# Kernel optimization log

Hardware: AMD Instinct MI355X
Metric: run time of the kernel (lower is better)

Reference implementation:

```python
import jax, jax.numpy as jnp
import numpy as np

B, SEQ, S, DIM_IN, DIM_K, DIM_V = 4, 2048, 128, 512, 64, 64
L = SEQ + 2 * S
NEG = -1e30  # stand-in for log(0) in the tril mask (finite for stable vjp)


def _layernorm(x, g, b, eps=1e-5):
    m = jnp.mean(x, axis=-1, keepdims=True)
    v = jnp.var(x, axis=-1, keepdims=True)
    return (x - m) / jnp.sqrt(v + eps) * g + b


def setup_inputs() -> dict:
    key = jax.random.key(0)
    ks = jax.random.split(key, 18)
    w = lambda k, shape, s=0.02: (jax.random.normal(k, shape, jnp.float32) * s)
    inp = {
        "x": jax.random.normal(ks[0], (B, L, DIM_IN), jnp.float32),
        "Wq": w(ks[1], (DIM_IN, DIM_K)),
        "Wk": w(ks[2], (DIM_IN, DIM_K)),
        "Wv": w(ks[3], (DIM_IN, DIM_V)),
        "Wq_s": w(ks[4], (DIM_IN, DIM_K)),
        "Wk_s": w(ks[5], (DIM_IN, DIM_K)),
        "Wv_s": w(ks[6], (DIM_IN, DIM_V)),
        "Wq_e": w(ks[7], (DIM_IN, DIM_K)),
        "Wk_e": w(ks[8], (DIM_IN, DIM_K)),
        "Wv_e": w(ks[9], (DIM_IN, DIM_V)),
        "ln_g": jnp.ones((DIM_IN,), jnp.float32),
        "ln_b": jnp.zeros((DIM_IN,), jnp.float32),
        "ln_s_g": jnp.ones((DIM_IN,), jnp.float32),
        "ln_s_b": jnp.zeros((DIM_IN,), jnp.float32),
        "ln_e_g": jnp.ones((DIM_IN,), jnp.float32),
        "ln_e_b": jnp.zeros((DIM_IN,), jnp.float32),
        "cope_emb": jax.random.normal(ks[10], (DIM_K, S), jnp.float32),
        "offset": 0,
    }
    return inp


def reference(x, Wq, Wk, Wv, Wq_s, Wk_s, Wv_s, Wq_e, Wk_e, Wv_e,
              ln_g, ln_b, ln_s_g, ln_s_b, ln_e_g, ln_e_b, cope_emb, offset):
    # extract_state: first/last state_len tokens
    xs, xm, xe = x[:, :S], x[:, S:L - S], x[:, -S:]
    xm = _layernorm(xm, ln_g, ln_b)
    xs = _layernorm(xs, ln_s_g, ln_s_b)
    xe = _layernorm(xe, ln_e_g, ln_e_b)

    q, k, v = xm @ Wq, xm @ Wk, xm @ Wv          # (B, SEQ, dk/dv)
    q_s, k_s, v_s = xs @ Wq_s, xs @ Wk_s, xs @ Wv_s
    q_e, k_e, v_e = xe @ Wq_e, xe @ Wk_e, xe @ Wv_e

    # CoPE bias over the non-state block
    logits = jnp.einsum('bqd,bkd->bqk', q, k)    # (B, SEQ, SEQ)
    gates = jax.nn.sigmoid(logits)
    pos = jnp.flip(jnp.cumsum(jnp.flip(gates, -1), axis=-1), -1)
    pos = jnp.minimum(pos, jnp.float32(S - 1))
    pos_ceil = jnp.ceil(pos).astype(jnp.int32)
    pos_floor = jnp.floor(pos).astype(jnp.int32)
    logits_int = jnp.einsum('bqd,dk->bqk', q, cope_emb)  # (B, SEQ, S)
    logits_c = jnp.take_along_axis(logits_int, pos_ceil, axis=-1)
    logits_f = jnp.take_along_axis(logits_int, pos_floor, axis=-1)
    wfrac = pos - pos_floor.astype(pos.dtype)
    bias = logits_c * wfrac + logits_f * (1.0 - wfrac)   # (B, SEQ, SEQ)

    q_full = jnp.concatenate([q_s, q, q_e], axis=1)      # (B, L, dk)
    k_full = jnp.concatenate([k_s, k, k_e], axis=1)
    v_full = jnp.concatenate([v_s, v, v_e], axis=1)

    # explicit tril log-mask bias with CoPE injected in the middle block
    tri = jnp.tril(jnp.ones((L, L), dtype=bool))
    attn_bias = jnp.where(tri, 0.0, NEG).astype(jnp.float32)
    attn_bias = jnp.broadcast_to(attn_bias, (B, L, L))
    attn_bias = attn_bias.at[:, S:L - S, S:L - S].add(bias)

    scale = 1.0 / jnp.sqrt(jnp.float32(DIM_K))
    scores = jnp.einsum('bqd,bkd->bqk', q_full, k_full) * scale + attn_bias
    att = jax.nn.softmax(scores, axis=-1)
    return jnp.einsum('bqk,bkd->bqd', att, v_full)       # (B, L, dv)
```

## Files before the change

kernel.cpp:

```cpp
#include <hip/hip_runtime.h>
#include <math.h>

#define B_    4
#define SEQ_  2048
#define S_    128
#define L_    2304
#define DIN   512
#define DK    64
#define NEGINF (-1e30f)
#define SCALE 0.125f
#define NCOLS 2176
#define NMID  8192
#define NEDGE 1024
#define LE    2304

typedef _Float16 f16;
typedef __attribute__((ext_vector_type(8))) _Float16 half8;
typedef __attribute__((ext_vector_type(4))) float f32x4;

union U4 { uint4 u; f16 h[8]; half8 v; };

__global__ __launch_bounds__(256) void k_wsplit(
    const float* __restrict__ Wq,  const float* __restrict__ Wk,  const float* __restrict__ Wv,
    const float* __restrict__ Wqs, const float* __restrict__ Wks, const float* __restrict__ Wvs,
    const float* __restrict__ Wqe, const float* __restrict__ Wke, const float* __restrict__ Wve,
    f16* __restrict__ Wsp)
{
    __shared__ float xs[64 * 68];
    const int kt  = blockIdx.x;
    const int mat = blockIdx.y;
    const float* W;
    switch (mat) {
        case 0: W = Wq;  break; case 1: W = Wk;  break; case 2: W = Wv;  break;
        case 3: W = Wqs; break; case 4: W = Wks; break; case 5: W = Wvs; break;
        case 6: W = Wqe; break; case 7: W = Wke; break; default: W = Wve; break;
    }
    const int tid = threadIdx.x;
    const int k0  = kt * 64;
    #pragma unroll
    for (int i = 0; i < 4; ++i) {
        int g = tid + 256 * i;
        int k = g >> 4, c4 = g & 15;
        *(float4*)(xs + k * 68 + c4 * 4) = ((const float4*)W)[(size_t)(k0 + k) * 16 + c4];
    }
    __syncthreads();
    const int col = tid & 63, hf = tid >> 6;
    const int kk0 = hf * 16;
    U4 hi0, hi1, lo0, lo1;
    #pragma unroll
    for (int j = 0; j < 8; ++j) {
        float v0 = xs[(kk0 + j) * 68 + col];
        float v1 = xs[(kk0 + 8 + j) * 68 + col];
        hi0.h[j] = (f16)v0; lo0.h[j] = (f16)(v0 - (float)hi0.h[j]);
        hi1.h[j] = (f16)v1; lo1.h[j] = (f16)(v1 - (float)hi1.h[j]);
    }
    f16* dst = Wsp + (size_t)mat * 65536 + (size_t)col * 1024 + k0 + kk0;
    *(uint4*)(dst)       = hi0.u;
    *(uint4*)(dst + 8)   = hi1.u;
    *(uint4*)(dst + 512) = lo0.u;
    *(uint4*)(dst + 520) = lo1.u;
}

__global__ __launch_bounds__(256) void k_proj(
    const float* __restrict__ x, const f16* __restrict__ Wsp,
    const float* __restrict__ g0, const float* __restrict__ b0,
    const float* __restrict__ gs, const float* __restrict__ bs,
    const float* __restrict__ ge, const float* __restrict__ be,
    f16* __restrict__ qsp, f16* __restrict__ ksp, f16* __restrict__ vhT)
{
    __shared__ f16 Bs[3 * 64 * 136];
    __shared__ float mean_s[32], rstd_s[32];
    const int tid  = threadIdx.x;
    const int row0 = blockIdx.x * 32;
    const int rseq = row0 % L_;
    const int seg  = (rseq < S_) ? 0 : (rseq >= L_ - S_) ? 2 : 1;
    const int mat0 = (seg == 0) ? 3 : (seg == 2) ? 6 : 0;
    const float* gg = (seg == 0) ? gs : (seg == 2) ? ge : g0;
    const float* bb = (seg == 0) ? bs : (seg == 2) ? be : b0;

    {
        const int rr = tid >> 3, qq = tid & 7;
        const float4* xr = (const float4*)(x + (size_t)(row0 + rr) * DIN) + qq * 16;
        float s = 0.f, s2 = 0.f;
        #pragma unroll
        for (int i = 0; i < 16; ++i) {
            float4 v = xr[i];
            s  += v.x + v.y + v.z + v.w;
            s2 += v.x * v.x + v.y * v.y + v.z * v.z + v.w * v.w;
        }
        s  += __shfl_xor(s, 1);  s  += __shfl_xor(s, 2);  s  += __shfl_xor(s, 4);
        s2 += __shfl_xor(s2, 1); s2 += __shfl_xor(s2, 2); s2 += __shfl_xor(s2, 4);
        if (qq == 0) {
            float mean = s * (1.f / DIN);
            mean_s[rr] = mean;
            rstd_s[rr] = rsqrtf(s2 * (1.f / DIN) - mean * mean + 1e-5f);
        }
    }

    const int w = tid >> 6, lane = tid & 63;
    const int cl = lane & 15, quad = lane >> 4;
    const int r0 = 16 * (w >> 1), c0 = 32 * (w & 1);

    f32x4 acc[3][2];
    #pragma unroll
    for (int m = 0; m < 3; ++m)
        #pragma unroll
        for (int j = 0; j < 2; ++j) acc[m][j] = 0.f;

    const int arow = row0 + r0 + cl;

    for (int kc = 0; kc < DIN; kc += 64) {
        __syncthreads();
        #pragma unroll
        for (int i = 0; i < 6; ++i) {
            int g = tid + 256 * i;
            int mm = g >> 9, rem = g & 511;
            int col = rem >> 3, c8 = rem & 7;
            const f16* src = Wsp + (size_t)(mat0 + mm) * 65536 + (size_t)col * 1024 + kc + c8 * 8;
            f16* dst = Bs + mm * 8704 + col * 136 + c8 * 8;
            *(uint4*)(dst)      = *(const uint4*)(src);
            *(uint4*)(dst + 64) = *(const uint4*)(src + 512);
        }
        __syncthreads();
        const float mean = mean_s[r0 + cl], rstd = rstd_s[r0 + cl];
        #pragma unroll
        for (int h = 0; h < 2; ++h) {
            const float* xp = x + (size_t)arow * DIN + kc + h * 32 + quad * 8;
            float4 a0 = *(const float4*)xp;
            float4 a1 = *(const float4*)(xp + 4);
            const float* gp = gg + kc + h * 32 + quad * 8;
            const float* bp = bb + kc + h * 32 + quad * 8;
            float4 gA = *(const float4*)gp, gB = *(const float4*)(gp + 4);
            float4 bA = *(const float4*)bp, bB = *(const float4*)(bp + 4);
            float n[8];
            n[0] = (a0.x - mean) * rstd * gA.x + bA.x;
            n[1] = (a0.y - mean) * rstd * gA.y + bA.y;
            n[2] = (a0.z - mean) * rstd * gA.z + bA.z;
            n[3] = (a0.w - mean) * rstd * gA.w + bA.w;
            n[4] = (a1.x - mean) * rstd * gB.x + bB.x;
            n[5] = (a1.y - mean) * rstd * gB.y + bB.y;
            n[6] = (a1.z - mean) * rstd * gB.z + bB.z;
            n[7] = (a1.w - mean) * rstd * gB.w + bB.w;
            U4 hi, lo;
            #pragma unroll
            for (int j = 0; j < 8; ++j) {
                hi.h[j] = (f16)n[j];
                lo.h[j] = (f16)(n[j] - (float)hi.h[j]);
            }
            half8 ah = hi.v, al = lo.v;
            #pragma unroll
            for (int m = 0; m < 3; ++m)
                #pragma unroll
                for (int cs = 0; cs < 2; ++cs) {
                    const f16* base = Bs + m * 8704 + (c0 + 16 * cs + cl) * 136 + h * 32 + quad * 8;
                    half8 bh = *(const half8*)(base);
                    half8 bl = *(const half8*)(base + 64);
                    acc[m][cs] = __builtin_amdgcn_mfma_f32_16x16x32_f16(ah, bh, acc[m][cs], 0, 0, 0);
                    acc[m][cs] = __builtin_amdgcn_mfma_f32_16x16x32_f16(ah, bl, acc[m][cs], 0, 0, 0);
                    acc[m][cs] = __builtin_amdgcn_mfma_f32_16x16x32_f16(al, bh, acc[m][cs], 0, 0, 0);
                }
        }
    }

    const int bI = row0 / L_;
    const int rb = row0 - bI * L_;
    #pragma unroll
    for (int m = 0; m < 3; ++m) {
        f16* sp = (m == 0) ? qsp : ksp;
        #pragma unroll
        for (int cs = 0; cs < 2; ++cs)
            #pragma unroll
            for (int r = 0; r < 4; ++r) {
                int lrow = r0 + quad * 4 + r;
                int col  = c0 + 16 * cs + cl;
                float v  = acc[m][cs][r];
                size_t grow = (size_t)(row0 + lrow);
                if (m < 2) {
                    f16 hv = (f16)v;
                    sp[grow * 128 + col]      = hv;
                    sp[grow * 128 + 64 + col] = (f16)(v - (float)hv);
                } else {
                    vhT[(size_t)(bI * 64 + col) * L_ + rb + lrow] = (f16)v;
                }
            }
    }
}

__global__ __launch_bounds__(256, 3) void k_dots(
    const f16* __restrict__ qsp, const f16* __restrict__ ksp,
    float* __restrict__ D32, float* __restrict__ G, float* __restrict__ De32)
{
    const int bx = blockIdx.x, by = blockIdx.y;
    const bool edge = (bx >= 64);
    int b, q0 = 0;
    size_t qrow0;
    if (!edge) {
        if (by >= 17) return;
        b = bx >> 4;
        q0 = (bx * 128) & 2047;
        qrow0 = (size_t)b * L_ + S_ + q0;
    } else {
        int ex = bx - 64;
        b = ex >> 1;
        int half = ex & 1;
        if (half == 0 && by > 0) return;
        qrow0 = (size_t)b * L_ + (half ? 2176 : 0);
    }
    const int col0 = by * 128;
    const size_t krow0 = (size_t)b * L_ + col0;

    __shared__ f16 Ks[128 * 136];
    const int tid = threadIdx.x;
    const int w = tid >> 6, lane = tid & 63;
    const int cl = lane & 15, quad = lane >> 4;

    half8 qh[2][2], qlo[2][2];
    #pragma unroll
    for (int rs = 0; rs < 2; ++rs)
        #pragma unroll
        for (int h = 0; h < 2; ++h) {
            const f16* qp = qsp + (qrow0 + 32 * w + 16 * rs + cl) * 128 + h * 32 + quad * 8;
            qh[rs][h]  = *(const half8*)qp;
            qlo[rs][h] = *(const half8*)(qp + 64);
        }

    #pragma unroll
    for (int i = 0; i < 8; ++i) {
        int g = tid + 256 * i;
        int r = g >> 4, c = g & 15;
        *(uint4*)(Ks + r * 136 + c * 8) = *(const uint4*)(ksp + (krow0 + r) * 128 + c * 8);
    }
    __syncthreads();

    f32x4 acc[2][8];
    #pragma unroll
    for (int i = 0; i < 2; ++i)
        #pragma unroll
        for (int j = 0; j < 8; ++j) acc[i][j] = 0.f;

    #pragma unroll
    for (int h = 0; h < 2; ++h) {
        #pragma unroll
        for (int cq = 0; cq < 2; ++cq) {
            half8 bh[4], bl[4];
            #pragma unroll
            for (int cc = 0; cc < 4; ++cc) {
                const f16* base = Ks + (16 * (cq * 4 + cc) + cl) * 136 + h * 32 + quad * 8;
                bh[cc] = *(const half8*)(base);
                bl[cc] = *(const half8*)(base + 64);
            }
            #pragma unroll
            for (int rs = 0; rs < 2; ++rs)
                #pragma unroll
                for (int cc = 0; cc < 4; ++cc) {
                    int c = cq * 4 + cc;
                    acc[rs][c] = __builtin_amdgcn_mfma_f32_16x16x32_f16(qh[rs][h], bh[cc], acc[rs][c], 0, 0, 0);
                    acc[rs][c] = __builtin_amdgcn_mfma_f32_16x16x32_f16(qh[rs][h], bl[cc], acc[rs][c], 0, 0, 0);
                    acc[rs][c] = __builtin_amdgcn_mfma_f32_16x16x32_f16(qlo[rs][h], bh[cc], acc[rs][c], 0, 0, 0);
                }
        }
    }

    if (!edge) {
        const int gr0 = bx * 128;
        const bool writeD = (by == 0) || ((by - 1) <= (q0 >> 7));
        if (writeD) {
            #pragma unroll
            for (int rs = 0; rs < 2; ++rs)
                #pragma unroll
                for (int c = 0; c < 8; ++c)
                    #pragma unroll
                    for (int r = 0; r < 4; ++r) {
                        int mrow = gr0 + 32 * w + 16 * rs + quad * 4 + r;
                        int n    = col0 + 16 * c + cl;
                        D32[(size_t)mrow * NCOLS + n] = acc[rs][c][r];
                    }
        }
        if (by >= 1) {
            const int chm = 2 * (by - 1);
            #pragma unroll
            for (int rs = 0; rs < 2; ++rs)
                #pragma unroll
                for (int r = 0; r < 4; ++r) {
                    float sA = 0.f, sB = 0.f;
                    #pragma unroll
                    for (int cc = 0; cc < 4; ++cc) {
                        sA += 1.f / (1.f + __expf(-acc[rs][cc][r]));
                        sB += 1.f / (1.f + __expf(-acc[rs][4 + cc][r]));
                    }
                    #pragma unroll
                    for (int off = 1; off < 16; off <<= 1) {
                        sA += __shfl_xor(sA, off);
                        sB += __shfl_xor(sB, off);
                    }
                    if (cl == 0) {
                        int row = gr0 + 32 * w + 16 * rs + quad * 4 + r;
                        G[(size_t)row * 32 + chm]     = sA;
                        G[(size_t)row * 32 + chm + 1] = sB;
                    }
                }
        }
    } else {
        const int er0 = (bx - 64) * 128;
        #pragma unroll
        for (int rs = 0; rs < 2; ++rs)
            #pragma unroll
            for (int c = 0; c < 8; ++c)
                #pragma unroll
                for (int r = 0; r < 4; ++r) {
                    int erow = er0 + 32 * w + 16 * rs + quad * 4 + r;
                    int n    = col0 + 16 * c + cl;
                    De32[(size_t)erow * LE + n] = acc[rs][c][r];
                }
    }
}

__global__ __launch_bounds__(256) void k_scan(
    const f16* __restrict__ qsp, const float* __restrict__ cope,
    const float* __restrict__ G,
    const float* __restrict__ D32, f16* __restrict__ Dp,
    const float* __restrict__ De32, f16* __restrict__ Dep)
{
    __shared__ f16   qvh[128];
    __shared__ float li[128];
    __shared__ float Gs[32];
    __shared__ float Gsf[32];
    __shared__ float wmax[4], wsum[4];
    const int tid = threadIdx.x;
    const int gr  = blockIdx.x;
    const int lane = tid & 63, wid = tid >> 6;

    if (gr < NMID) {
        const int b = gr >> 11;
        const int q = gr & 2047;
        const size_t grow = (size_t)b * L_ + S_ + q;
        const int qlim = (q & ~63) + 64;

        if (tid < 16) ((uint4*)qvh)[tid] = ((const uint4*)(qsp + grow * 128))[tid];
        if (tid >= 16 && tid < 24)
            ((float4*)Gs)[tid - 16] = ((const float4*)G)[(size_t)gr * 8 + tid - 16];
        __syncthreads();
        if (tid < 128) {
            float a = 0.f;
            #pragma unroll
            for (int d = 0; d < DK; ++d)
                a += ((float)qvh[d] + (float)qvh[64 + d]) * cope[d * S_ + tid];
            li[tid] = a;
        }
        if (tid >= 128 && tid < 160) {
            int c = tid - 128;
            float s = 0.f;
            for (int cc = c + 1; cc < 32; ++cc) s += Gs[cc];
            Gsf[c] = s;
        }

        const float* Sr = D32 + (size_t)gr * NCOLS;
        f16* Dr = Dp + (size_t)gr * NCOLS;
        const int j0 = tid * 8;
        const int cg = tid >> 3, sl = tid & 7;
        float dot[8], gte[8];
        float csum = 0.f;
        if (j0 < qlim) {
            float4 t0 = *(const float4*)(Sr + 128 + j0);
            float4 t1 = *(const float4*)(Sr + 128 + j0 + 4);
            dot[0] = t0.x; dot[1] = t0.y; dot[2] = t0.z; dot[3] = t0.w;
            dot[4] = t1.x; dot[5] = t1.y; dot[6] = t1.z; dot[7] = t1.w;
            #pragma unroll
            for (int jj = 0; jj < 8; ++jj) {
                gte[jj] = 1.f / (1.f + __expf(-dot[jj]));
                csum += gte[jj];
            }
        } else {
            #pragma unroll
            for (int jj = 0; jj < 8; ++jj) { dot[jj] = 0.f; gte[jj] = 0.f; }
        }
        float sv = (tid < 128) ? Sr[tid] * SCALE : NEGINF;

        float inc = csum;
        #pragma unroll
        for (int off = 1; off < 8; off <<= 1) {
            float u = __shfl_down(inc, off, 8);
            if (sl + off < 8) inc += u;
        }
        __syncthreads();
        float run = (inc - csum) + Gsf[cg];

        float p8[8];
        #pragma unroll
        for (int jj = 7; jj >= 0; --jj) {
            run += gte[jj];
            float pos = fminf(run, (float)(S_ - 1));
            float pfl = floorf(pos);
            int ic  = (int)ceilf(pos);
            int ifl = (int)pfl;
            float w = pos - pfl;
            float bias = li[ic] * w + li[ifl] * (1.f - w);
            p8[jj] = (j0 + jj <= q) ? dot[jj] * SCALE + bias : NEGINF;
        }

        float mx = sv;
        #pragma unroll
        for (int jj = 0; jj < 8; ++jj) mx = fmaxf(mx, p8[jj]);
        #pragma unroll
        for (int off = 1; off < 64; off <<= 1) mx = fmaxf(mx, __shfl_xor(mx, off));
        if (lane == 0) wmax[wid] = mx;
        __syncthreads();
        mx = fmaxf(fmaxf(wmax[0], wmax[1]), fmaxf(wmax[2], wmax[3]));

        float lsum = 0.f;
        float e8[8];
        #pragma unroll
        for (int jj = 0; jj < 8; ++jj) {
            e8[jj] = __expf(p8[jj] - mx);
            lsum += e8[jj];
        }
        float es = 0.f;
        if (tid < 128) { es = __expf(sv - mx); lsum += es; }
        #pragma unroll
        for (int off = 1; off < 64; off <<= 1) lsum += __shfl_xor(lsum, off);
        if (lane == 0) wsum[wid] = lsum;
        __syncthreads();
        float inv = 1.f / (wsum[0] + wsum[1] + wsum[2] + wsum[3]);

        if (j0 < qlim) {
            U4 o;
            #pragma unroll
            for (int jj = 0; jj < 8; ++jj) o.h[jj] = (f16)(e8[jj] * inv);
            *(uint4*)(Dr + 128 + j0) = o.u;
        }
        if (tid < 128) Dr[tid] = (f16)(es * inv);
    } else {
        const int er = gr - NMID;
        const int r  = er & 255;
        const int Q  = (r < 128) ? r : (2048 + r);
        const float* Er32 = De32 + (size_t)er * LE;
        f16* Er = Dep + (size_t)er * LE;

        float v[9];
        #pragma unroll
        for (int i = 0; i < 9; ++i) {
            int j = tid + 256 * i;
            float d = Er32[j];
            v[i] = (j <= Q) ? d * SCALE : NEGINF;
        }
        float mx = v[0];
        #pragma unroll
        for (int i = 1; i < 9; ++i) mx = fmaxf(mx, v[i]);
        #pragma unroll
        for (int off = 1; off < 64; off <<= 1) mx = fmaxf(mx, __shfl_xor(mx, off));
        if (lane == 0) wmax[wid] = mx;
        __syncthreads();
        mx = fmaxf(fmaxf(wmax[0], wmax[1]), fmaxf(wmax[2], wmax[3]));

        float lsum = 0.f;
        #pragma unroll
        for (int i = 0; i < 9; ++i) {
            v[i] = __expf(v[i] - mx);
            lsum += v[i];
        }
        #pragma unroll
        for (int off = 1; off < 64; off <<= 1) lsum += __shfl_xor(lsum, off);
        if (lane == 0) wsum[wid] = lsum;
        __syncthreads();
        float inv = 1.f / (wsum[0] + wsum[1] + wsum[2] + wsum[3]);

        #pragma unroll
        for (int i = 0; i < 9; ++i)
            Er[tid + 256 * i] = (f16)(v[i] * inv);
    }
}

__global__ __launch_bounds__(512) void k_pv(
    const f16* __restrict__ Pmid, const f16* __restrict__ Pedge,
    const f16* __restrict__ vhT, float* __restrict__ out)
{
    __shared__ float mbuf[3][2][16 * 68];
    const int tid = threadIdx.x, bx = blockIdx.x;
    const int w = tid >> 6, lane = tid & 63;
    const int cl = lane & 15, quad = lane >> 4;
    const int g = w >> 2, ql = w & 3;
    const bool edge = (bx >= 256);

    const f16* Pb;
    size_t prow0, pitch;
    int b, cmax, cap, q0 = 0, r0 = 0;
    if (!edge) {
        int gr0 = bx * 32;
        b = gr0 >> 11; q0 = gr0 & 2047;
        Pb = Pmid; prow0 = gr0; pitch = NCOLS; cap = 34;
        cmax = (159 + q0) >> 6;
    } else {
        int er0 = (bx - 256) * 32;
        b = er0 >> 8; r0 = er0 & 255;
        Pb = Pedge; prow0 = er0; pitch = LE; cap = 36;
        int Qmax = (r0 < 128) ? (r0 + 31) : (2048 + r0 + 31);
        cmax = Qmax >> 6;
    }
    int c_end = cmax + 1;
    if (c_end > cap) c_end = cap;

    f32x4 acc[4];
    #pragma unroll
    for (int c = 0; c < 4; ++c) acc[c] = 0.f;

    for (int ch = ql; ch < c_end; ch += 4) {
        #pragma unroll
        for (int h = 0; h < 2; ++h) {
            half8 pa = *(const half8*)(Pb + (prow0 + 16 * g + cl) * pitch + ch * 64 + h * 32 + quad * 8);
            #pragma unroll
            for (int c2 = 0; c2 < 4; ++c2) {
                half8 bv = *(const half8*)(vhT + (size_t)(b * 64 + 16 * c2 + cl) * L_ + ch * 64 + h * 32 + quad * 8);
                acc[c2] = __builtin_amdgcn_mfma_f32_16x16x32_f16(pa, bv, acc[c2], 0, 0, 0);
            }
        }
    }

    if (ql != 0) {
        #pragma unroll
        for (int c2 = 0; c2 < 4; ++c2)
            #pragma unroll
            for (int r = 0; r < 4; ++r)
                mbuf[ql - 1][g][(quad * 4 + r) * 68 + 16 * c2 + cl] = acc[c2][r];
    }
    __syncthreads();
    if (ql == 0) {
        #pragma unroll
        for (int c2 = 0; c2 < 4; ++c2)
            #pragma unroll
            for (int r = 0; r < 4; ++r) {
                int idx = (quad * 4 + r) * 68 + 16 * c2 + cl;
                float v = acc[c2][r] + mbuf[0][g][idx] + mbuf[1][g][idx] + mbuf[2][g][idx];
                int lrow = 16 * g + quad * 4 + r;
                size_t grow;
                if (!edge) {
                    grow = (size_t)b * L_ + S_ + q0 + lrow;
                } else {
                    int rr = r0 + lrow;
                    int gQ = (rr < 128) ? rr : (2048 + rr);
                    grow = (size_t)b * L_ + gQ;
                }
                out[grow * DK + 16 * c2 + cl] = v;
            }
    }
}

extern "C" void kernel_launch(void* const* d_in, const int* in_sizes, int n_in,
                              void* d_out, int out_size, void* d_ws, size_t ws_size,
                              hipStream_t stream)
{
    const float* x    = (const float*)d_in[0];
    const float* Wq   = (const float*)d_in[1];
    const float* Wk   = (const float*)d_in[2];
    const float* Wv   = (const float*)d_in[3];
    const float* Wqs  = (const float*)d_in[4];
    const float* Wks  = (const float*)d_in[5];
    const float* Wvs  = (const float*)d_in[6];
    const float* Wqe  = (const float*)d_in[7];
    const float* Wke  = (const float*)d_in[8];
    const float* Wve  = (const float*)d_in[9];
    const float* g0   = (const float*)d_in[10];
    const float* b0   = (const float*)d_in[11];
    const float* gs   = (const float*)d_in[12];
    const float* bs   = (const float*)d_in[13];
    const float* ge   = (const float*)d_in[14];
    const float* be   = (const float*)d_in[15];
    const float* cope = (const float*)d_in[16];

    const size_t NR = (size_t)B_ * L_;
    f16*   qsp   = (f16*)d_ws;
    f16*   ksp   = qsp + NR * 128;
    f16*   vhT   = ksp + NR * 128;
    f16*   Wsp   = vhT + NR * 64;
    float* G     = (float*)(Wsp + (size_t)9 * 65536);
    float* Dm32  = G + (size_t)NMID * 32;
    float* De32  = Dm32 + (size_t)NMID * NCOLS;
    f16*   Dp    = (f16*)(De32 + (size_t)NEDGE * LE);
    f16*   Dep   = Dp + (size_t)NMID * NCOLS;
    float* out   = (float*)d_out;

    k_wsplit<<<dim3(8, 9), 256, 0, stream>>>(Wq, Wk, Wv, Wqs, Wks, Wvs,
                                             Wqe, Wke, Wve, Wsp);
    k_proj<<<288, 256, 0, stream>>>(x, Wsp, g0, b0, gs, bs, ge, be,
                                    qsp, ksp, vhT);
    k_dots<<<dim3(72, 18), 256, 0, stream>>>(qsp, ksp, Dm32, G, De32);
    k_scan<<<NMID + NEDGE, 256, 0, stream>>>(qsp, cope, G, Dm32, Dp, De32, Dep);
    k_pv<<<288, 512, 0, stream>>>(Dp, Dep, vhT, out);
}
```

Measured before the change: 229.1 us.

## Restructure projection kernel: stage normalized rows in LDS, read weights directly from global

The projection kernel now handles 16 rows per block instead of 32, doubling the grid to 576 blocks. The layernormed and hi/lo-split activations are written once into shared memory, and each wave computes 48 output columns across the three weight matrices, reading the split weights straight from global/L2 with no LDS staging. This removes the per-chunk weight copy and its barriers and improves parallelism on a small kernel. In exchange, weight reuse drops, global weight traffic per block rises, and it relies on L2 hits.

```diff
diff --git a/kernel.cpp b/kernel.cpp
--- a/kernel.cpp
+++ b/kernel.cpp
@@ -68,10 +68,10 @@
     const float* __restrict__ ge, const float* __restrict__ be,
     f16* __restrict__ qsp, f16* __restrict__ ksp, f16* __restrict__ vhT)
 {
-    __shared__ f16 Bs[3 * 64 * 136];
-    __shared__ float mean_s[32], rstd_s[32];
+    __shared__ f16 As[16 * 1032];
+    __shared__ float mean_s[16], rstd_s[16];
     const int tid  = threadIdx.x;
-    const int row0 = blockIdx.x * 32;
+    const int row0 = blockIdx.x * 16;
     const int rseq = row0 % L_;
     const int seg  = (rseq < S_) ? 0 : (rseq >= L_ - S_) ? 2 : 1;
     const int mat0 = (seg == 0) ? 3 : (seg == 2) ? 6 : 0;
@@ -79,57 +79,38 @@
     const float* bb = (seg == 0) ? bs : (seg == 2) ? be : b0;
 
     {
-        const int rr = tid >> 3, qq = tid & 7;
-        const float4* xr = (const float4*)(x + (size_t)(row0 + rr) * DIN) + qq * 16;
+        const int rr = tid >> 4, qq = tid & 15;
+        const float4* xr = (const float4*)(x + (size_t)(row0 + rr) * DIN) + qq * 8;
         float s = 0.f, s2 = 0.f;
         #pragma unroll
-        for (int i = 0; i < 16; ++i) {
+        for (int i = 0; i < 8; ++i) {
             float4 v = xr[i];
             s  += v.x + v.y + v.z + v.w;
             s2 += v.x * v.x + v.y * v.y + v.z * v.z + v.w * v.w;
         }
-        s  += __shfl_xor(s, 1);  s  += __shfl_xor(s, 2);  s  += __shfl_xor(s, 4);
-        s2 += __shfl_xor(s2, 1); s2 += __shfl_xor(s2, 2); s2 += __shfl_xor(s2, 4);
+        s  += __shfl_xor(s, 1);  s  += __shfl_xor(s, 2);
+        s  += __shfl_xor(s, 4);  s  += __shfl_xor(s, 8);
+        s2 += __shfl_xor(s2, 1); s2 += __shfl_xor(s2, 2);
+        s2 += __shfl_xor(s2, 4); s2 += __shfl_xor(s2, 8);
         if (qq == 0) {
             float mean = s * (1.f / DIN);
             mean_s[rr] = mean;
             rstd_s[rr] = rsqrtf(s2 * (1.f / DIN) - mean * mean + 1e-5f);
         }
     }
-
-    const int w = tid >> 6, lane = tid & 63;
-    const int cl = lane & 15, quad = lane >> 4;
-    const int r0 = 16 * (w >> 1), c0 = 32 * (w & 1);
-
-    f32x4 acc[3][2];
-    #pragma unroll
-    for (int m = 0; m < 3; ++m)
-        #pragma unroll
-        for (int j = 0; j < 2; ++j) acc[m][j] = 0.f;
-
-    const int arow = row0 + r0 + cl;
-
-    for (int kc = 0; kc < DIN; kc += 64) {
-        __syncthreads();
-        #pragma unroll
-        for (int i = 0; i < 6; ++i) {
-            int g = tid + 256 * i;
-            int mm = g >> 9, rem = g & 511;
-            int col = rem >> 3, c8 = rem & 7;
-            const f16* src = Wsp + (size_t)(mat0 + mm) * 65536 + (size_t)col * 1024 + kc + c8 * 8;
-            f16* dst = Bs + mm * 8704 + col * 136 + c8 * 8;
-            *(uint4*)(dst)      = *(const uint4*)(src);
-            *(uint4*)(dst + 64) = *(const uint4*)(src + 512);
-        }
-        __syncthreads();
-        const float mean = mean_s[r0 + cl], rstd = rstd_s[r0 + cl];
-        #pragma unroll
-        for (int h = 0; h < 2; ++h) {
-            const float* xp = x + (size_t)arow * DIN + kc + h * 32 + quad * 8;
+    __syncthreads();
+
+    {
+        const int r = tid >> 4, c32 = (tid & 15) * 32;
+        const float mean = mean_s[r], rstd = rstd_s[r];
+        f16* dst = As + r * 1032 + c32;
+        #pragma unroll
+        for (int i = 0; i < 4; ++i) {
+            const float* xp = x + (size_t)(row0 + r) * DIN + c32 + i * 8;
             float4 a0 = *(const float4*)xp;
             float4 a1 = *(const float4*)(xp + 4);
-            const float* gp = gg + kc + h * 32 + quad * 8;
-            const float* bp = bb + kc + h * 32 + quad * 8;
+            const float* gp = gg + c32 + i * 8;
+            const float* bp = bb + c32 + i * 8;
             float4 gA = *(const float4*)gp, gB = *(const float4*)(gp + 4);
             float4 bA = *(const float4*)bp, bB = *(const float4*)(bp + 4);
             float n[8];
@@ -147,42 +128,62 @@
                 hi.h[j] = (f16)n[j];
                 lo.h[j] = (f16)(n[j] - (float)hi.h[j]);
             }
-            half8 ah = hi.v, al = lo.v;
-            #pragma unroll
-            for (int m = 0; m < 3; ++m)
-                #pragma unroll
-                for (int cs = 0; cs < 2; ++cs) {
-                    const f16* base = Bs + m * 8704 + (c0 + 16 * cs + cl) * 136 + h * 32 + quad * 8;
-                    half8 bh = *(const half8*)(base);
-                    half8 bl = *(const half8*)(base + 64);
-                    acc[m][cs] = __builtin_amdgcn_mfma_f32_16x16x32_f16(ah, bh, acc[m][cs], 0, 0, 0);
-                    acc[m][cs] = __builtin_amdgcn_mfma_f32_16x16x32_f16(ah, bl, acc[m][cs], 0, 0, 0);
-                    acc[m][cs] = __builtin_amdgcn_mfma_f32_16x16x32_f16(al, bh, acc[m][cs], 0, 0, 0);
-                }
+            *(uint4*)(dst + i * 8)       = hi.u;
+            *(uint4*)(dst + 512 + i * 8) = lo.u;
+        }
+    }
+    __syncthreads();
+
+    const int w = tid >> 6, lane = tid & 63;
+    const int cl = lane & 15, quad = lane >> 4;
+
+    const f16* bptr[3];
+    #pragma unroll
+    for (int j = 0; j < 3; ++j) {
+        int C = 48 * w + 16 * j + cl;
+        bptr[j] = Wsp + (size_t)(mat0 + (C >> 6)) * 65536 + (size_t)(C & 63) * 1024;
+    }
+
+    f32x4 acc[3];
+    #pragma unroll
+    for (int j = 0; j < 3; ++j) acc[j] = 0.f;
+
+    #pragma unroll
+    for (int ks = 0; ks < 16; ++ks) {
+        const int k0 = ks * 32 + quad * 8;
+        half8 ah = *(const half8*)(As + cl * 1032 + k0);
+        half8 al = *(const half8*)(As + cl * 1032 + 512 + k0);
+        #pragma unroll
+        for (int j = 0; j < 3; ++j) {
+            half8 bh = *(const half8*)(bptr[j] + k0);
+            half8 bl = *(const half8*)(bptr[j] + 512 + k0);
+            acc[j] = __builtin_amdgcn_mfma_f32_16x16x32_f16(ah, bh, acc[j], 0, 0, 0);
+            acc[j] = __builtin_amdgcn_mfma_f32_16x16x32_f16(ah, bl, acc[j], 0, 0, 0);
+            acc[j] = __builtin_amdgcn_mfma_f32_16x16x32_f16(al, bh, acc[j], 0, 0, 0);
         }
     }
 
     const int bI = row0 / L_;
     const int rb = row0 - bI * L_;
     #pragma unroll
-    for (int m = 0; m < 3; ++m) {
-        f16* sp = (m == 0) ? qsp : ksp;
-        #pragma unroll
-        for (int cs = 0; cs < 2; ++cs)
-            #pragma unroll
-            for (int r = 0; r < 4; ++r) {
-                int lrow = r0 + quad * 4 + r;
-                int col  = c0 + 16 * cs + cl;
-                float v  = acc[m][cs][r];
-                size_t grow = (size_t)(row0 + lrow);
-                if (m < 2) {
-                    f16 hv = (f16)v;
-                    sp[grow * 128 + col]      = hv;
-                    sp[grow * 128 + 64 + col] = (f16)(v - (float)hv);
-                } else {
-                    vhT[(size_t)(bI * 64 + col) * L_ + rb + lrow] = (f16)v;
-                }
+    for (int j = 0; j < 3; ++j) {
+        const int cb   = 48 * w + 16 * j;
+        const int mat  = cb >> 6;
+        const int mcol = (cb & 63) + cl;
+        #pragma unroll
+        for (int r = 0; r < 4; ++r) {
+            int lrow = quad * 4 + r;
+            float v  = acc[j][r];
+            size_t grow = (size_t)(row0 + lrow);
+            if (mat < 2) {
+                f16* sp = (mat == 0) ? qsp : ksp;
+                f16 hv = (f16)v;
+                sp[grow * 128 + mcol]      = hv;
+                sp[grow * 128 + 64 + mcol] = (f16)(v - (float)hv);
+            } else {
+                vhT[(size_t)(bI * 64 + mcol) * L_ + rb + lrow] = (f16)v;
             }
+        }
     }
 }
 
@@ -580,7 +581,7 @@
 
     k_wsplit<<<dim3(8, 9), 256, 0, stream>>>(Wq, Wk, Wv, Wqs, Wks, Wvs,
                                              Wqe, Wke, Wve, Wsp);
-    k_proj<<<288, 256, 0, stream>>>(x, Wsp, g0, b0, gs, bs, ge, be,
+    k_proj<<<576, 256, 0, stream>>>(x, Wsp, g0, b0, gs, bs, ge, be,
                                     qsp, ksp, vhT);
     k_dots<<<dim3(72, 18), 256, 0, stream>>>(qsp, ksp, Dm32, G, De32);
     k_scan<<<NMID + NEDGE, 256, 0, stream>>>(qsp, cope, G, Dm32, Dp, De32, Dep);
```

Result: no change. 225.1 us (-1.8%).
